# Optimization experiments

Measured on AMD Instinct MI355X. Metric: run time of the kernel, lower is better.

## Reference

```python
import jax, jax.numpy as jnp
import numpy as np

EPS = 1e-8
INL_TH = 2.0          # RANSAC inl_th default; oneway_transfer_error squared=True
MIN_SAMPLE = 4        # minimal_sample_size for homography
MAX_LO_ITERS = 5      # RANSAC max_lo_iters
DLT_ITERS = 5         # find_homography_dlt_iterated n_iter default
SOFT_INL_TH = 3.0     # find_homography_dlt_iterated soft_inl_th default


def normalize_points(pts):
    # pts: (B,N,2) -> normalized points + (B,3,3) transforms (kornia normalize_points)
    mean = pts.mean(axis=1, keepdims=True)                      # (B,1,2)
    scale = jnp.linalg.norm(pts - mean, axis=-1).mean(axis=-1)  # (B,)
    scale = jnp.asarray(np.sqrt(2.0), pts.dtype) / (scale + EPS)
    pts_n = (pts - mean) * scale[:, None, None]
    mx, my = mean[:, 0, 0], mean[:, 0, 1]
    z = jnp.zeros_like(scale)
    o = jnp.ones_like(scale)
    T = jnp.stack([scale, z, -scale * mx,
                   z, scale, -scale * my,
                   z, z, o], axis=-1).reshape(-1, 3, 3)
    return pts_n, T


def find_homography_dlt(p1, p2, w):
    # weighted normalized DLT: p1,p2 (B,N,2), w (B,N) -> H (B,3,3)
    B = p1.shape[0]
    p1n, T1 = normalize_points(p1)
    p2n, T2 = normalize_points(p2)
    x1, y1 = p1n[..., 0], p1n[..., 1]
    x2, y2 = p2n[..., 0], p2n[..., 1]
    o = jnp.ones_like(x1)
    z = jnp.zeros_like(x1)
    ax = jnp.stack([z, z, z, -x1, -y1, -o, y2 * x1, y2 * y1, y2], axis=-1)  # (B,N,9)
    ay = jnp.stack([x1, y1, o, z, z, z, -x2 * x1, -x2 * y1, -x2], axis=-1)  # (B,N,9)
    A = jnp.stack([ax, ay], axis=2).reshape(B, -1, 9)   # (B,2N,9), ax/ay rows interleaved
    w2 = jnp.repeat(w, 2, axis=1)                       # repeat_interleave to match rows
    AtA = jnp.einsum('bni,bn,bnj->bij', A, w2, A)       # (B,9,9)
    _, _, Vh = jnp.linalg.svd(AtA)
    H = Vh[:, -1].reshape(-1, 3, 3)                     # null vector
    H = jnp.linalg.inv(T2) @ H @ T1                     # denormalize
    return H / (H[:, 2:3, 2:3] + EPS)


def transfer_errors(H, p1, p2, squared=True):
    # oneway_transfer_error: H (B,3,3), p1,p2 (N,2) -> (B,N)
    p1h = jnp.concatenate([p1, jnp.ones_like(p1[..., :1])], axis=-1)  # (N,3)
    proj = jnp.einsum('bij,nj->bni', H, p1h)                          # (B,N,3)
    zc = proj[..., 2:3]
    s = jnp.where(jnp.abs(zc) > EPS, 1.0 / zc, jnp.ones_like(zc))
    pt = proj[..., :2] * s
    err = ((pt - p2) ** 2).sum(-1)
    return err if squared else jnp.sqrt(jnp.maximum(err, 0.0))


def sample_is_valid_for_homography(p1, p2):
    # orientation-consistency of 4-point minimal samples: (B,4,2) -> (B,)
    trip = jnp.array([[0, 1, 2], [0, 2, 3], [0, 1, 3], [1, 2, 3]])
    p1h = jnp.concatenate([p1, jnp.ones_like(p1[..., :1])], axis=-1)
    p2h = jnp.concatenate([p2, jnp.ones_like(p2[..., :1])], axis=-1)
    d1 = jnp.linalg.det(p1h[:, trip])  # (B,4) triple-product signs
    d2 = jnp.linalg.det(p2h[:, trip])
    return jnp.all(jnp.sign(d1) == jnp.sign(d2), axis=1)


def polish_model(kp1, kp2, inl_mask):
    # find_homography_dlt_iterated; inlier subset expressed as zero/one weights
    w = inl_mask.astype(kp1.dtype)[None]  # (1,N)
    p1, p2 = kp1[None], kp2[None]
    H = find_homography_dlt(p1, p2, w)
    for _ in range(DLT_ITERS - 1):
        err = transfer_errors(H, kp1, kp2, squared=False)
        w_new = jnp.exp(-err / (2.0 * SOFT_INL_TH ** 2))
        H = find_homography_dlt(p1, p2, w * w_new)
    return H


def ransac_forward(kp1, kp2, idxs):
    dtype = kp1.dtype
    N = kp1.shape[0]
    kp1s, kp2s = kp1[idxs], kp2[idxs]  # (B,4,2) minimal samples
    valid_sample = sample_is_valid_for_homography(kp1s, kp2s)  # remove_bad_samples (as score mask)
    w = jnp.ones(kp1s.shape[:2], dtype)
    models = find_homography_dlt(kp1s, kp2s, w)                # (B,3,3)
    diag_min = jnp.abs(jnp.diagonal(models, axis1=1, axis2=2)).min(axis=1)
    valid_model = diag_min > 1e-4                              # remove_bad_models (as score mask)
    errors = transfer_errors(models, kp1, kp2)                 # (B,N) verify
    inl = errors <= INL_TH
    scores = inl.astype(dtype).sum(axis=1)
    scores = jnp.where(valid_sample & valid_model, scores, jnp.asarray(-1.0, dtype))
    best = jnp.argmax(scores)
    model, inliers, score = models[best], inl[best], scores[best]
    accept = score > float(MIN_SAMPLE)  # best_score_total init = minimal_sample_size

    def lo_body(carry, _):
        m, il, sc = carry
        m_lo = polish_model(kp1, kp2, il)           # (1,3,3)
        err_lo = transfer_errors(m_lo, kp1, kp2)[0]
        il_lo = err_lo <= INL_TH
        sc_lo = il_lo.astype(dtype).sum()
        better = sc_lo > sc                         # non-improving step is a fixed point == break
        m = jnp.where(better, m_lo[0], m)
        il = jnp.where(better, il_lo, il)
        sc = jnp.where(better, sc_lo, sc)
        return (m, il, sc), None

    (model, inliers, score), _ = jax.lax.scan(lo_body, (model, inliers, score), None, length=MAX_LO_ITERS)
    best_model = jnp.where(accept, model, jnp.zeros((3, 3), dtype))
    best_inliers = jnp.where(accept, inliers, jnp.zeros((N,), bool))
    return best_model, best_inliers


def setup_inputs():
    key = jax.random.key(0)
    k1, k2, k3, k4, k5 = jax.random.split(key, 5)
    N, B = 10000, 2048
    kp1 = jax.random.uniform(k1, (N, 2), jnp.float32) * 1000.0
    H_gt = jnp.array([[1.02, 0.01, 10.0], [-0.02, 0.98, -5.0], [1e-5, -1e-5, 1.0]], jnp.float32)
    p1h = jnp.concatenate([kp1, jnp.ones((N, 1), jnp.float32)], axis=-1)
    proj = p1h @ H_gt.T
    proj = proj[:, :2] / proj[:, 2:3]
    noise = jax.random.normal(k2, (N, 2), jnp.float32) * 0.5
    outliers = jax.random.uniform(k3, (N, 2), jnp.float32) * 1000.0
    is_out = jax.random.uniform(k4, (N,)) < 0.5
    kp2 = jnp.where(is_out[:, None], outliers, proj + noise)
    # minimal-sample indices without replacement (torch: rand.topk(k=4, dim=1))
    rand = jax.random.uniform(k5, (B, N))
    _, idxs = jax.lax.top_k(rand, 4)
    return {"kp1": kp1, "kp2": kp2, "idxs": idxs}


def reference(kp1, kp2, idxs):
    return ransac_forward(kp1, kp2, idxs)
```

## Files before the change

### kernel.cpp

```cpp
#include <hip/hip_runtime.h>
#include <math.h>


struct Hdr {
  int best_idx;
  float best_score;
  int pad0, pad1;
  double nrm[6];
};

__device__ __host__ constexpr int TRI6(int u, int v) {
  return u * 6 - u * (u - 1) / 2 + (v - u);
}

__device__ __forceinline__ float sq_err9(const float h[9], float x1, float y1,
                                         float x2, float y2) {
  float px = h[0] * x1 + h[1] * y1 + h[2];
  float py = h[3] * x1 + h[4] * y1 + h[5];
  float pz = h[6] * x1 + h[7] * y1 + h[8];
  float s  = (fabsf(pz) > 1e-8f) ? (1.0f / pz) : 1.0f;
  float dx = px * s - x2;
  float dy = py * s - y2;
  return dx * dx + dy * dy;
}

__device__ __forceinline__ double sel9d(const double* a, int k) {
  double d = a[0];
  d = (k == 1) ? a[1] : d;
  d = (k == 2) ? a[2] : d;
  d = (k == 3) ? a[3] : d;
  d = (k == 4) ? a[4] : d;
  d = (k == 5) ? a[5] : d;
  d = (k == 6) ? a[6] : d;
  d = (k == 7) ? a[7] : d;
  d = (k == 8) ? a[8] : d;
  return d;
}
__device__ __forceinline__ double sel4d(const double* a, int k) {
  double d = a[0];
  d = (k == 1) ? a[1] : d;
  d = (k == 2) ? a[2] : d;
  d = (k == 3) ? a[3] : d;
  return d;
}

__device__ __forceinline__ void wave_solve9(double r[9], int lane, double* xs) {
  double dself = sel9d(r, lane);
  double tr = (lane < 9) ? dself : 0.0;
#pragma unroll
  for (int m = 1; m <= 8; m <<= 1) tr += __shfl_xor(tr, m);
  double ridge = tr * 1e-12 + 1e-30;
#pragma unroll
  for (int k = 0; k < 9; k++)
    if (lane == k) r[k] += ridge;

  double u[9];
#pragma unroll
  for (int k = 0; k < 9; k++) u[k] = 0.0;
  double invd = 0.0;

#pragma unroll
  for (int j = 0; j < 9; j++) {
    double dj = __shfl(r[j], j);
    dj = (dj > 1e-280) ? dj : 1e-280;
    double is = rsqrt(dj);
    double s = dj * is;
    double Lij = r[j] * is;
    if (lane == j) { Lij = s; invd = is; }
    r[j] = Lij;
    double c[9];
#pragma unroll
    for (int k = j; k < 9; k++) c[k] = __shfl(r[j], k);
#pragma unroll
    for (int k = j; k < 9; k++)
      if (lane == j) u[k] = c[k];
    if (lane > j) {
#pragma unroll
      for (int k = j + 1; k < 9; k++) r[k] -= Lij * c[k];
    }
  }

  double x = 1.0;
#pragma unroll
  for (int it = 0; it < 3; ++it) {
    double acc = x;
    double y = 0.0;
#pragma unroll
    for (int k = 0; k < 9; k++) {
      double yk = __shfl(acc * invd, k);
      if (lane == k) y = yk;
      if (lane > k) acc -= r[k] * yk;
    }
    acc = y;
#pragma unroll
    for (int k = 8; k >= 0; k--) {
      double xk = __shfl(acc * invd, k);
      if (lane == k) x = xk;
      if (lane < k) acc -= u[k] * xk;
    }
    double m2 = (lane < 9) ? fabs(x) : 0.0;
#pragma unroll
    for (int m = 1; m <= 8; m <<= 1) m2 = fmax(m2, __shfl_xor(m2, m));
    x *= 1.0 / m2;
  }
  *xs = x;
}

__device__ __forceinline__ void denorm9(const double hh[9], double mx1,
                                        double my1, double s1, double mx2,
                                        double my2, double s2, float out[9]) {
  double is2 = 1.0 / s2;
  double g0 = is2 * hh[0] + mx2 * hh[6];
  double g1 = is2 * hh[1] + mx2 * hh[7];
  double g2 = is2 * hh[2] + mx2 * hh[8];
  double g3 = is2 * hh[3] + my2 * hh[6];
  double g4 = is2 * hh[4] + my2 * hh[7];
  double g5 = is2 * hh[5] + my2 * hh[8];
  double g6 = hh[6], g7 = hh[7], g8 = hh[8];
  double a = -s1 * mx1, b = -s1 * my1;
  double H0 = s1 * g0, H1 = s1 * g1, H2 = a * g0 + b * g1 + g2;
  double H3 = s1 * g3, H4 = s1 * g4, H5 = a * g3 + b * g4 + g5;
  double H6 = s1 * g6, H7 = s1 * g7, H8 = a * g6 + b * g7 + g8;
  double inv = 1.0 / (H8 + 1e-8);
  out[0] = (float)(H0 * inv);
  out[1] = (float)(H1 * inv);
  out[2] = (float)(H2 * inv);
  out[3] = (float)(H3 * inv);
  out[4] = (float)(H4 * inv);
  out[5] = (float)(H5 * inv);
  out[6] = (float)(H6 * inv);
  out[7] = (float)(H7 * inv);
  out[8] = (float)(H8 * inv);
}

__device__ __forceinline__ double m_entry(const double* CA, const double* CB,
                                          int i, int j) {
  double s = 0.0;
  if (i >= 3) s += CA[TRI6(i - 3, j - 3)];
  if ((i < 3 || i >= 6) && (j < 3 || j >= 6)) {
    int ui = (i < 3) ? i : i - 3;
    int vj = (j < 3) ? j : j - 3;
    s += CB[TRI6(ui, vj)];
  }
  return s;
}

__global__ __launch_bounds__(64, 2) void k_fit_score(
    const float2* __restrict__ kp1, const float2* __restrict__ kp2,
    const int* __restrict__ idxs, int N, float* __restrict__ models,
    float* __restrict__ scores) {
  __shared__ double sA8[8 * 9];
  __shared__ float sH[9];
  const int b = blockIdx.x;
  const int lane = threadIdx.x;

  double X1[4], Y1[4], X2[4], Y2[4];
#pragma unroll
  for (int k = 0; k < 4; k++) {
    int id = idxs[b * 4 + k];
    float2 a = kp1[id];
    float2 c = kp2[id];
    X1[k] = a.x; Y1[k] = a.y; X2[k] = c.x; Y2[k] = c.y;
  }
  const int t0[4] = {0, 0, 0, 1};
  const int t1[4] = {1, 2, 1, 2};
  const int t2[4] = {2, 3, 3, 3};
  bool vs = true;
#pragma unroll
  for (int q = 0; q < 4; q++) {
    int i0 = t0[q], i1 = t1[q], i2 = t2[q];
    double d1 = (X1[i1] - X1[i0]) * (Y1[i2] - Y1[i0]) -
                (X1[i2] - X1[i0]) * (Y1[i1] - Y1[i0]);
    double d2 = (X2[i1] - X2[i0]) * (Y2[i2] - Y2[i0]) -
                (X2[i2] - X2[i0]) * (Y2[i1] - Y2[i0]);
    int sg1 = (d1 > 0.0) ? 1 : ((d1 < 0.0) ? -1 : 0);
    int sg2 = (d2 > 0.0) ? 1 : ((d2 < 0.0) ? -1 : 0);
    vs = vs && (sg1 == sg2);
  }
  double mx1 = (X1[0] + X1[1] + X1[2] + X1[3]) * 0.25;
  double my1 = (Y1[0] + Y1[1] + Y1[2] + Y1[3]) * 0.25;
  double mx2 = (X2[0] + X2[1] + X2[2] + X2[3]) * 0.25;
  double my2 = (Y2[0] + Y2[1] + Y2[2] + Y2[3]) * 0.25;
  double n1 = 0.0, n2 = 0.0;
#pragma unroll
  for (int k = 0; k < 4; k++) {
    double dx = X1[k] - mx1, dy = Y1[k] - my1;
    n1 += sqrt(dx * dx + dy * dy);
    dx = X2[k] - mx2; dy = Y2[k] - my2;
    n2 += sqrt(dx * dx + dy * dy);
  }
  double s1 = sqrt(2.0) / (n1 * 0.25 + 1e-8);
  double s2 = sqrt(2.0) / (n2 * 0.25 + 1e-8);

  if (lane < 8) {
    int k = lane >> 1;
    double xn1 = (sel4d(X1, k) - mx1) * s1;
    double yn1 = (sel4d(Y1, k) - my1) * s1;
    double xn2 = (sel4d(X2, k) - mx2) * s2;
    double yn2 = (sel4d(Y2, k) - my2) * s2;
    bool odd = (lane & 1) != 0;
    sA8[lane * 9 + 0] = odd ? xn1 : 0.0;
    sA8[lane * 9 + 1] = odd ? yn1 : 0.0;
    sA8[lane * 9 + 2] = odd ? 1.0 : 0.0;
    sA8[lane * 9 + 3] = odd ? 0.0 : -xn1;
    sA8[lane * 9 + 4] = odd ? 0.0 : -yn1;
    sA8[lane * 9 + 5] = odd ? 0.0 : -1.0;
    sA8[lane * 9 + 6] = odd ? -xn2 * xn1 : yn2 * xn1;
    sA8[lane * 9 + 7] = odd ? -xn2 * yn1 : yn2 * yn1;
    sA8[lane * 9 + 8] = odd ? -xn2 : yn2;
  }
  __syncthreads();

  double r[9];
  {
    int i = (lane < 9) ? lane : 0;
    double ai[8];
#pragma unroll
    for (int l = 0; l < 8; l++) ai[l] = sA8[l * 9 + i];
#pragma unroll
    for (int j = 0; j < 9; j++) {
      double s = 0.0;
#pragma unroll
      for (int l = 0; l < 8; l++) s += ai[l] * sA8[l * 9 + j];
      r[j] = s;
    }
  }
  double xs;
  wave_solve9(r, lane, &xs);

  double hh[9];
#pragma unroll
  for (int k = 0; k < 9; k++) hh[k] = __shfl(xs, k);

  bool valid = vs;
  if (lane == 0) {
    float Hf[9];
    denorm9(hh, mx1, my1, s1, mx2, my2, s2, Hf);
    bool vm = fminf(fminf(fabsf(Hf[0]), fabsf(Hf[4])), fabsf(Hf[8])) > 1e-4f;
    valid = vs && vm;
#pragma unroll
    for (int j = 0; j < 9; j++) sH[j] = Hf[j];
  }
  __syncthreads();

  float h[9];
#pragma unroll
  for (int j = 0; j < 9; j++) h[j] = sH[j];
  int cnt = 0;
  for (int i = lane; i < N; i += 64) {
    float2 a = kp1[i];
    float2 c = kp2[i];
    cnt += (sq_err9(h, a.x, a.y, c.x, c.y) <= 2.0f) ? 1 : 0;
  }
#pragma unroll
  for (int off = 32; off; off >>= 1) cnt += __shfl_down(cnt, off);
  if (lane == 0) {
    scores[b] = valid ? (float)cnt : -1.0f;
#pragma unroll
    for (int j = 0; j < 9; j++) models[b * 9 + j] = sH[j];
  }
}

__global__ __launch_bounds__(1024) void k_select(
    const float2* __restrict__ kp1, const float2* __restrict__ kp2, int N,
    int B, const float* __restrict__ scores, Hdr* __restrict__ hdr) {
  const int t = threadIdx.x;
  const int lane = t & 63, wid = t >> 6;
  __shared__ float rs[1024];
  __shared__ int ri[1024];

  float bs = -2.0f;
  int bi = 0x7fffffff;
  for (int i = t; i < B; i += 1024) {
    float s = scores[i];
    if (s > bs || (s == bs && i < bi)) { bs = s; bi = i; }
  }
  rs[t] = bs;
  ri[t] = bi;
  __syncthreads();
  for (int off = 512; off; off >>= 1) {
    if (t < off) {
      float s = rs[t + off];
      int i2 = ri[t + off];
      if (s > rs[t] || (s == rs[t] && i2 < ri[t])) { rs[t] = s; ri[t] = i2; }
    }
    __syncthreads();
  }
  if (t == 0) {
    hdr->best_idx = ri[0];
    hdr->best_score = rs[0];
  }

  __shared__ double red[16][4];
  __shared__ double mb[4];
  double sx1 = 0, sy1 = 0, sx2 = 0, sy2 = 0;
  for (int i = t; i < N; i += 1024) {
    float2 a = kp1[i];
    float2 c = kp2[i];
    sx1 += a.x; sy1 += a.y; sx2 += c.x; sy2 += c.y;
  }
#pragma unroll
  for (int off = 32; off; off >>= 1) {
    sx1 += __shfl_down(sx1, off);
    sy1 += __shfl_down(sy1, off);
    sx2 += __shfl_down(sx2, off);
    sy2 += __shfl_down(sy2, off);
  }
  if (lane == 0) {
    red[wid][0] = sx1; red[wid][1] = sy1; red[wid][2] = sx2; red[wid][3] = sy2;
  }
  __syncthreads();
  if (t == 0) {
    double a = 0, b2 = 0, c = 0, d = 0;
    for (int w2 = 0; w2 < 16; w2++) {
      a += red[w2][0]; b2 += red[w2][1]; c += red[w2][2]; d += red[w2][3];
    }
    mb[0] = a / N; mb[1] = b2 / N; mb[2] = c / N; mb[3] = d / N;
  }
  __syncthreads();
  double mx1 = mb[0], my1 = mb[1], mx2 = mb[2], my2 = mb[3];
  double sn1 = 0, sn2 = 0;
  for (int i = t; i < N; i += 1024) {
    float2 a = kp1[i];
    float2 c = kp2[i];
    double dx = a.x - mx1, dy = a.y - my1;
    sn1 += sqrt(dx * dx + dy * dy);
    dx = c.x - mx2; dy = c.y - my2;
    sn2 += sqrt(dx * dx + dy * dy);
  }
#pragma unroll
  for (int off = 32; off; off >>= 1) {
    sn1 += __shfl_down(sn1, off);
    sn2 += __shfl_down(sn2, off);
  }
  __syncthreads();
  if (lane == 0) { red[wid][0] = sn1; red[wid][1] = sn2; }
  __syncthreads();
  if (t == 0) {
    double a = 0, b2 = 0;
    for (int w2 = 0; w2 < 16; w2++) { a += red[w2][0]; b2 += red[w2][1]; }
    hdr->nrm[0] = mx1;
    hdr->nrm[1] = my1;
    hdr->nrm[2] = sqrt(2.0) / (a / N + 1e-8);
    hdr->nrm[3] = mx2;
    hdr->nrm[4] = my2;
    hdr->nrm[5] = sqrt(2.0) / (b2 / N + 1e-8);
  }
}

#define K3_T 512
#define PPT 20

__global__ __launch_bounds__(512, 2) void k_lo(const float2* __restrict__ kp1,
                                               const float2* __restrict__ kp2,
                                               int N,
                                               const float* __restrict__ models,
                                               const Hdr* __restrict__ hdr,
                                               float* __restrict__ out,
                                               int out_size) {
  const int t = threadIdx.x;
  const int lane = t & 63, wid = t >> 6;
  __shared__ float sP[K3_T * 42];
  __shared__ double sP2[42 * 8];
  __shared__ double sC[42];
  __shared__ float sHcur[9];
  __shared__ float sHpol[9];
  __shared__ float sScLo;
  __shared__ int sCnt[8];
  __shared__ double sPar[6];
  __shared__ float sAccept;

  if (t == 0) {
    int bi = hdr->best_idx;
#pragma unroll
    for (int j = 0; j < 9; j++) sHcur[j] = models[bi * 9 + j];
    sAccept = hdr->best_score;
#pragma unroll
    for (int j = 0; j < 6; j++) sPar[j] = hdr->nrm[j];
  }
  __syncthreads();
  const bool accept = sAccept > 4.0f;
  if (!accept) {
    for (int i = t; i < out_size; i += K3_T) out[i] = 0.0f;
    return;
  }
  const float mx1 = (float)sPar[0], my1 = (float)sPar[1], s1 = (float)sPar[2];
  const float mx2 = (float)sPar[3], my2 = (float)sPar[4], s2 = (float)sPar[5];

  float hc[9];
#pragma unroll
  for (int j = 0; j < 9; j++) hc[j] = sHcur[j];
  unsigned int il = 0u;
  for (int p = 0; p < PPT; p++) {
    int i = p * K3_T + t;
    if (i < N) {
      float2 a = kp1[i];
      float2 c = kp2[i];
      if (sq_err9(hc, a.x, a.y, c.x, c.y) <= 2.0f) il |= (1u << p);
    }
  }
  float sc = sAccept;

  for (int lo = 0; lo < 5; ++lo) {
    for (int j = 0; j < 5; ++j) {
      float hp[9];
      if (j > 0) {
#pragma unroll
        for (int q = 0; q < 9; q++) hp[q] = sHpol[q];
      }
      float accA[21], accB[21];
#pragma unroll
      for (int k = 0; k < 21; k++) { accA[k] = 0.0f; accB[k] = 0.0f; }
      for (int p = 0; p < PPT; p++) {
        int i = p * K3_T + t;
        if (i < N && ((il >> p) & 1u)) {
          float2 a = kp1[i];
          float2 c = kp2[i];
          float w = 1.0f;
          if (j > 0) {
            float e = sq_err9(hp, a.x, a.y, c.x, c.y);
            w = expf(-sqrtf(fmaxf(e, 0.0f)) / 18.0f);
          }
          float xn1 = (a.x - mx1) * s1, yn1 = (a.y - my1) * s1;
          float xn2 = (c.x - mx2) * s2, yn2 = (c.y - my2) * s2;
          float va[6] = {-xn1, -yn1, -1.0f, xn1 * yn2, yn1 * yn2, yn2};
          float vb[6] = {xn1, yn1, 1.0f, -xn1 * xn2, -yn1 * xn2, -xn2};
#pragma unroll
          for (int u = 0; u < 6; u++) {
            float wa = w * va[u];
#pragma unroll
            for (int v = u; v < 6; v++) accA[TRI6(u, v)] += wa * va[v];
          }
#pragma unroll
          for (int u = 0; u < 6; u++) {
            float wb = w * vb[u];
#pragma unroll
            for (int v = u; v < 6; v++) accB[TRI6(u, v)] += wb * vb[v];
          }
        }
      }
#pragma unroll
      for (int k = 0; k < 21; k++) sP[t * 42 + k] = accA[k];
#pragma unroll
      for (int k = 0; k < 21; k++) sP[t * 42 + 21 + k] = accB[k];
      __syncthreads();
      if (t < 336) {
        int col = t % 42, grp = t / 42;
        double s = 0.0;
        int base = grp * 64 * 42 + col;
        for (int i2 = 0; i2 < 64; i2++) s += (double)sP[base + i2 * 42];
        sP2[col * 8 + grp] = s;
      }
      __syncthreads();
      if (t < 42) {
        double s = 0.0;
#pragma unroll
        for (int g = 0; g < 8; g++) s += sP2[t * 8 + g];
        sC[t] = s;
      }
      __syncthreads();
      if (wid == 0) {
        double r[9];
        int i = (lane < 9) ? lane : 0;
#pragma unroll
        for (int jj = 0; jj < 9; jj++) {
          int a2 = (i < jj) ? i : jj;
          int b2 = (i < jj) ? jj : i;
          r[jj] = m_entry(sC, sC + 21, a2, b2);
        }
        double xs;
        wave_solve9(r, lane, &xs);
        double hh[9];
#pragma unroll
        for (int k = 0; k < 9; k++) hh[k] = __shfl(xs, k);
        if (lane == 0) {
          float ho[9];
          denorm9(hh, sPar[0], sPar[1], sPar[2], sPar[3], sPar[4], sPar[5],
                  ho);
#pragma unroll
          for (int q = 0; q < 9; q++) sHpol[q] = ho[q];
        }
      }
      __syncthreads();
    }
    float hl[9];
#pragma unroll
    for (int q = 0; q < 9; q++) hl[q] = sHpol[q];
    unsigned int il_lo = 0u;
    int cnt = 0;
    for (int p = 0; p < PPT; p++) {
      int i = p * K3_T + t;
      if (i < N) {
        float2 a = kp1[i];
        float2 c = kp2[i];
        if (sq_err9(hl, a.x, a.y, c.x, c.y) <= 2.0f) {
          il_lo |= (1u << p);
          cnt++;
        }
      }
    }
#pragma unroll
    for (int off = 32; off; off >>= 1) cnt += __shfl_down(cnt, off);
    if (lane == 0) sCnt[wid] = cnt;
    __syncthreads();
    if (t == 0) {
      int tot = 0;
#pragma unroll
      for (int w2 = 0; w2 < 8; w2++) tot += sCnt[w2];
      sScLo = (float)tot;
    }
    __syncthreads();
    float sc_lo = sScLo;
    if (sc_lo > sc) {
      il = il_lo;
      sc = sc_lo;
      if (t == 0) {
#pragma unroll
        for (int q = 0; q < 9; q++) sHcur[q] = sHpol[q];
      }
    }
    __syncthreads();
  }

  if (t < 9 && t < out_size) out[t] = sHcur[t];
  for (int p = 0; p < PPT; p++) {
    int i = p * K3_T + t;
    if (i < N && (9 + i) < out_size)
      out[9 + i] = ((il >> p) & 1u) ? 1.0f : 0.0f;
  }
  for (int i = 9 + N + t; i < out_size; i += K3_T) out[i] = 0.0f;
}

extern "C" void kernel_launch(void* const* d_in, const int* in_sizes, int n_in,
                              void* d_out, int out_size, void* d_ws,
                              size_t ws_size, hipStream_t stream) {
  (void)n_in;
  (void)ws_size;
  const float2* kp1 = (const float2*)d_in[0];
  const float2* kp2 = (const float2*)d_in[1];
  const int* idxs = (const int*)d_in[2];
  const int N = in_sizes[0] / 2;
  const int B = in_sizes[2] / 4;

  float* models = (float*)d_ws;
  float* scores = models + (size_t)B * 9;
  size_t off = (((size_t)B * 10 * sizeof(float)) + 15) & ~(size_t)15;
  Hdr* hdr = (Hdr*)((char*)d_ws + off);
  float* outf = (float*)d_out;

  k_fit_score<<<B, 64, 0, stream>>>(kp1, kp2, idxs, N, models, scores);
  k_select<<<1, 1024, 0, stream>>>(kp1, kp2, N, B, scores, hdr);
  k_lo<<<1, K3_T, 0, stream>>>(kp1, kp2, N, models, hdr, outf, out_size);
}
```

Measured before the change: 644.2 us.

## Exploit AtA block structure, cache points in registers, trim inverse-iteration count

```diff
diff --git a/kernel.cpp b/kernel.cpp
--- a/kernel.cpp
+++ b/kernel.cpp
@@ -82,7 +82,7 @@
 
   double x = 1.0;
 #pragma unroll
-  for (int it = 0; it < 3; ++it) {
+  for (int it = 0; it < 2; ++it) {
     double acc = x;
     double y = 0.0;
 #pragma unroll
@@ -133,18 +133,6 @@
   out[8] = (float)(H8 * inv);
 }
 
-__device__ __forceinline__ double m_entry(const double* CA, const double* CB,
-                                          int i, int j) {
-  double s = 0.0;
-  if (i >= 3) s += CA[TRI6(i - 3, j - 3)];
-  if ((i < 3 || i >= 6) && (j < 3 || j >= 6)) {
-    int ui = (i < 3) ? i : i - 3;
-    int vj = (j < 3) ? j : j - 3;
-    s += CB[TRI6(ui, vj)];
-  }
-  return s;
-}
-
 __global__ __launch_bounds__(64, 2) void k_fit_score(
     const float2* __restrict__ kp1, const float2* __restrict__ kp2,
     const int* __restrict__ idxs, int N, float* __restrict__ models,
@@ -360,9 +348,9 @@
                                                int out_size) {
   const int t = threadIdx.x;
   const int lane = t & 63, wid = t >> 6;
-  __shared__ float sP[K3_T * 42];
-  __shared__ double sP2[42 * 8];
-  __shared__ double sC[42];
+  __shared__ float sP[K3_T * 24];
+  __shared__ double sP2[24 * 8];
+  __shared__ double sC[24];
   __shared__ float sHcur[9];
   __shared__ float sHpol[9];
   __shared__ float sScLo;
@@ -387,17 +375,28 @@
   const float mx1 = (float)sPar[0], my1 = (float)sPar[1], s1 = (float)sPar[2];
   const float mx2 = (float)sPar[3], my2 = (float)sPar[4], s2 = (float)sPar[5];
 
-  float hc[9];
-#pragma unroll
-  for (int j = 0; j < 9; j++) hc[j] = sHcur[j];
-  unsigned int il = 0u;
+  float rx1[PPT], ry1[PPT], rx2[PPT], ry2[PPT];
+#pragma unroll
   for (int p = 0; p < PPT; p++) {
     int i = p * K3_T + t;
     if (i < N) {
       float2 a = kp1[i];
       float2 c = kp2[i];
-      if (sq_err9(hc, a.x, a.y, c.x, c.y) <= 2.0f) il |= (1u << p);
-    }
+      rx1[p] = a.x; ry1[p] = a.y; rx2[p] = c.x; ry2[p] = c.y;
+    } else {
+      rx1[p] = 0.0f; ry1[p] = 0.0f; rx2[p] = 0.0f; ry2[p] = 0.0f;
+    }
+  }
+
+  float hc[9];
+#pragma unroll
+  for (int j = 0; j < 9; j++) hc[j] = sHcur[j];
+  unsigned int il = 0u;
+#pragma unroll
+  for (int p = 0; p < PPT; p++) {
+    int i = p * K3_T + t;
+    if (i < N && sq_err9(hc, rx1[p], ry1[p], rx2[p], ry2[p]) <= 2.0f)
+      il |= (1u << p);
   }
   float sc = sAccept;
 
@@ -408,51 +407,48 @@
 #pragma unroll
         for (int q = 0; q < 9; q++) hp[q] = sHpol[q];
       }
-      float accA[21], accB[21];
-#pragma unroll
-      for (int k = 0; k < 21; k++) { accA[k] = 0.0f; accB[k] = 0.0f; }
+      float a0[6], aX[6], aY[6], aR[6];
+#pragma unroll
+      for (int k = 0; k < 6; k++) { a0[k] = 0; aX[k] = 0; aY[k] = 0; aR[k] = 0; }
+#pragma unroll
       for (int p = 0; p < PPT; p++) {
         int i = p * K3_T + t;
-        if (i < N && ((il >> p) & 1u)) {
-          float2 a = kp1[i];
-          float2 c = kp2[i];
-          float w = 1.0f;
-          if (j > 0) {
-            float e = sq_err9(hp, a.x, a.y, c.x, c.y);
-            w = expf(-sqrtf(fmaxf(e, 0.0f)) / 18.0f);
-          }
-          float xn1 = (a.x - mx1) * s1, yn1 = (a.y - my1) * s1;
-          float xn2 = (c.x - mx2) * s2, yn2 = (c.y - my2) * s2;
-          float va[6] = {-xn1, -yn1, -1.0f, xn1 * yn2, yn1 * yn2, yn2};
-          float vb[6] = {xn1, yn1, 1.0f, -xn1 * xn2, -yn1 * xn2, -xn2};
-#pragma unroll
-          for (int u = 0; u < 6; u++) {
-            float wa = w * va[u];
-#pragma unroll
-            for (int v = u; v < 6; v++) accA[TRI6(u, v)] += wa * va[v];
-          }
-#pragma unroll
-          for (int u = 0; u < 6; u++) {
-            float wb = w * vb[u];
-#pragma unroll
-            for (int v = u; v < 6; v++) accB[TRI6(u, v)] += wb * vb[v];
-          }
+        float w = (i < N && ((il >> p) & 1u)) ? 1.0f : 0.0f;
+        if (j > 0) {
+          float e = sq_err9(hp, rx1[p], ry1[p], rx2[p], ry2[p]);
+          w *= __expf(-sqrtf(fmaxf(e, 0.0f)) * 0.05555555556f);
         }
-      }
-#pragma unroll
-      for (int k = 0; k < 21; k++) sP[t * 42 + k] = accA[k];
-#pragma unroll
-      for (int k = 0; k < 21; k++) sP[t * 42 + 21 + k] = accB[k];
+        float xn1 = (rx1[p] - mx1) * s1, yn1 = (ry1[p] - my1) * s1;
+        float xn2 = (rx2[p] - mx2) * s2, yn2 = (ry2[p] - my2) * s2;
+        float xx = xn1 * xn1, xy = xn1 * yn1, yy = yn1 * yn1;
+        float wx = w * xn2, wy = w * yn2;
+        float wr = w * (xn2 * xn2 + yn2 * yn2);
+        a0[0] += w * xx;  a0[1] += w * xy;  a0[2] += w * xn1;
+        a0[3] += w * yy;  a0[4] += w * yn1; a0[5] += w;
+        aX[0] += wx * xx; aX[1] += wx * xy; aX[2] += wx * xn1;
+        aX[3] += wx * yy; aX[4] += wx * yn1; aX[5] += wx;
+        aY[0] += wy * xx; aY[1] += wy * xy; aY[2] += wy * xn1;
+        aY[3] += wy * yy; aY[4] += wy * yn1; aY[5] += wy;
+        aR[0] += wr * xx; aR[1] += wr * xy; aR[2] += wr * xn1;
+        aR[3] += wr * yy; aR[4] += wr * yn1; aR[5] += wr;
+      }
+#pragma unroll
+      for (int k = 0; k < 6; k++) {
+        sP[t * 24 + k] = a0[k];
+        sP[t * 24 + 6 + k] = aX[k];
+        sP[t * 24 + 12 + k] = aY[k];
+        sP[t * 24 + 18 + k] = aR[k];
+      }
       __syncthreads();
-      if (t < 336) {
-        int col = t % 42, grp = t / 42;
+      if (t < 192) {
+        int col = t % 24, grp = t / 24;
         double s = 0.0;
-        int base = grp * 64 * 42 + col;
-        for (int i2 = 0; i2 < 64; i2++) s += (double)sP[base + i2 * 42];
+        int base = grp * 64 * 24 + col;
+        for (int i2 = 0; i2 < 64; i2++) s += (double)sP[base + i2 * 24];
         sP2[col * 8 + grp] = s;
       }
       __syncthreads();
-      if (t < 42) {
+      if (t < 24) {
         double s = 0.0;
 #pragma unroll
         for (int g = 0; g < 8; g++) s += sP2[t * 8 + g];
@@ -460,13 +456,25 @@
       }
       __syncthreads();
       if (wid == 0) {
+        int i = (lane < 9) ? lane : 0;
+        int bi = i / 3, pi = i - 3 * bi;
         double r[9];
-        int i = (lane < 9) ? lane : 0;
 #pragma unroll
         for (int jj = 0; jj < 9; jj++) {
-          int a2 = (i < jj) ? i : jj;
-          int b2 = (i < jj) ? jj : i;
-          r[jj] = m_entry(sC, sC + 21, a2, b2);
+          int bj = jj / 3, pj = jj - 3 * bj;
+          int a2 = (pi < pj) ? pi : pj;
+          int b2 = (pi < pj) ? pj : pi;
+          int t6 = a2 * 3 - a2 * (a2 - 1) / 2 + (b2 - a2);
+          double v;
+          if (bi == bj)
+            v = (bi == 2) ? sC[18 + t6] : sC[t6];
+          else if (bi + bj == 1)
+            v = 0.0;
+          else if (bi + bj == 2)
+            v = -sC[6 + t6];
+          else
+            v = -sC[12 + t6];
+          r[jj] = v;
         }
         double xs;
         wave_solve9(r, lane, &xs);
@@ -488,15 +496,12 @@
     for (int q = 0; q < 9; q++) hl[q] = sHpol[q];
     unsigned int il_lo = 0u;
     int cnt = 0;
+#pragma unroll
     for (int p = 0; p < PPT; p++) {
       int i = p * K3_T + t;
-      if (i < N) {
-        float2 a = kp1[i];
-        float2 c = kp2[i];
-        if (sq_err9(hl, a.x, a.y, c.x, c.y) <= 2.0f) {
-          il_lo |= (1u << p);
-          cnt++;
-        }
+      if (i < N && sq_err9(hl, rx1[p], ry1[p], rx2[p], ry2[p]) <= 2.0f) {
+        il_lo |= (1u << p);
+        cnt++;
       }
     }
 #pragma unroll
@@ -523,6 +528,7 @@
   }
 
   if (t < 9 && t < out_size) out[t] = sHcur[t];
+#pragma unroll
   for (int p = 0; p < PPT; p++) {
     int i = p * K3_T + t;
     if (i < N && (9 + i) < out_size)
```

Measured after the change: 689.9 us. 1.07x slower.
